# Kernel optimization log

Hardware: AMD Instinct MI355X
Metric: run time of the kernel (lower is better)

## Reference

```python
import jax, jax.numpy as jnp
import numpy as np

D_ATT = 1024
N_HEADS = 16
D_HEAD = D_ATT // N_HEADS


def _xavier(key, shape, scale):
    # xavier_uniform for Linear(d, d): limit = sqrt(6/(fan_in+fan_out))
    limit = float(np.sqrt(6.0 / (shape[0] + shape[1])))
    return jax.random.uniform(key, shape, jnp.float32, -limit, limit) * scale


def setup_inputs() -> dict:
    key = jax.random.key(0)
    ks = jax.random.split(key, 7)
    B, Lt, Ls = 2, 2048, 2048
    s = 1.0 / np.sqrt(D_ATT)
    return {
        "x_target": jax.random.normal(ks[0], (B, Lt, D_ATT), jnp.float32),
        "x_source": jax.random.normal(ks[1], (B, Ls, D_ATT), jnp.float32),
        "Wq": _xavier(ks[2], (D_ATT, D_ATT), s),  # torch Linear weight [out, in]
        "Wk": _xavier(ks[3], (D_ATT, D_ATT), s),
        "Wv": _xavier(ks[4], (D_ATT, D_ATT), s),
        "Wo": _xavier(ks[5], (D_ATT, D_ATT), 1.0),
        "bo": jax.random.uniform(ks[6], (D_ATT,), jnp.float32, -s, s),
    }


def reference(x_target, x_source, Wq, Wk, Wv, Wo, bo):
    B, Lt, _ = x_target.shape
    Ls = x_source.shape[1]
    H, Dh = N_HEADS, D_HEAD
    # projections (torch Linear: x @ W^T); RoPE defaults to identity
    Q = (x_target @ Wq.T).reshape(B, Lt, H, Dh)  # [B, Lt, H, Dh]
    K = (x_source @ Wk.T).reshape(B, Ls, H, Dh)
    V = (x_source @ Wv.T).reshape(B, Ls, H, Dh)
    scores = jnp.einsum("bthd,bshd->bhts", Q, K) / np.sqrt(Dh)
    attn = jax.nn.softmax(scores, axis=-1)
    out = jnp.einsum("bhts,bshd->bthd", attn, V).reshape(B, Lt, H * Dh)
    return out @ Wo.T + bo  # dropout p=0 -> identity
```

## Files before the change

### kernel.cpp

```cpp
#include <hip/hip_runtime.h>
#include <hip/hip_bf16.h>

typedef short bf16x8 __attribute__((ext_vector_type(8)));
typedef float f32x4 __attribute__((ext_vector_type(4)));

#define LDP 72

__device__ __forceinline__ float bf2f(ushort u) {
    union { unsigned int i; float f; } v; v.i = ((unsigned int)u) << 16; return v.f;
}
__device__ __forceinline__ ushort f2bf(float f) {
    union { float f; unsigned int i; } v; v.f = f;
    unsigned int x = v.i;
    x += 0x7fffu + ((x >> 16) & 1u);
    return (ushort)(x >> 16);
}

#define MFMA(a, b, c) __builtin_amdgcn_mfma_f32_16x16x32_bf16(a, b, c, 0, 0, 0)

__device__ __forceinline__ void gld_lds16(const ushort* g, ushort* l) {
    __builtin_amdgcn_global_load_lds(
        (const __attribute__((address_space(1))) unsigned int*)g,
        (__attribute__((address_space(3))) unsigned int*)l, 16, 0, 0);
}

#define WS_XT 0
#define WS_XS 4194304
#define WS_WQ 8388608
#define WS_WK 9437184
#define WS_WV 10485760
#define WS_WO 11534336
#define WS_QH 12582912
#define WS_KH 16777216
#define WS_VT 20971520
#define WS_AO 0

__global__ __launch_bounds__(256) void cast_bf16(
    const float* __restrict__ s0, const float* __restrict__ s1,
    const float* __restrict__ s2, const float* __restrict__ s3,
    const float* __restrict__ s4, const float* __restrict__ s5,
    ushort* __restrict__ ws)
{
    const int seg = blockIdx.y;
    const float* src = seg == 0 ? s0 : seg == 1 ? s1 : seg == 2 ? s2
                     : seg == 3 ? s3 : seg == 4 ? s4 : s5;
    const size_t off = seg == 0 ? WS_XT : seg == 1 ? WS_XS : seg == 2 ? WS_WQ
                     : seg == 3 ? WS_WK : seg == 4 ? WS_WV : (size_t)WS_WO;
    const int n4 = (seg < 2) ? 1048576 : 262144;
    ushort* d = ws + off;
    for (int i = blockIdx.x * 256 + threadIdx.x; i < n4; i += gridDim.x * 256) {
        float4 f = ((const float4*)src)[i];
        ushort4 u;
        u.x = f2bf(f.x); u.y = f2bf(f.y); u.z = f2bf(f.z); u.w = f2bf(f.w);
        ((ushort4*)d)[i] = u;
    }
}

__global__ __launch_bounds__(256) void gemm128(
    const ushort* __restrict__ xtb, const ushort* __restrict__ xsb,
    const ushort* __restrict__ wqb, const ushort* __restrict__ wkb,
    const ushort* __restrict__ wvb,
    ushort* __restrict__ qh, ushort* __restrict__ kh, ushort* __restrict__ vt)
{
    __shared__ __align__(16) ushort SM[16384];

    const int mode = blockIdx.z;
    const ushort* Ap = (mode == 0) ? xtb : xsb;
    const ushort* Wp = (mode == 0) ? wqb : (mode == 1 ? wkb : wvb);

    const int tid  = threadIdx.x;
    const int wave = tid >> 6, lane = tid & 63;
    const int quad = lane >> 4, lidx = lane & 15;
    const int wm = wave >> 1, wn = wave & 1;
    const int m0 = blockIdx.y * 128, n0 = blockIdx.x * 128;

    const int slr = lane >> 2, scb = lane & 3;
    auto stage = [&](int k0, int bufi) {
        ushort* Asb = SM + bufi * 4096;
        ushort* Bsb = SM + 8192 + bufi * 4096;
#pragma unroll
        for (int i2 = 0; i2 < 2; ++i2) {
            const int i = wave + i2 * 4;
            const int r = i * 16 + slr;
            gld_lds16(Ap + (size_t)(m0 + r) * 1024 + k0 + scb * 8, Asb + i * 512);
            gld_lds16(Wp + (size_t)(n0 + r) * 1024 + k0 + scb * 8, Bsb + i * 512);
        }
    };

    f32x4 acc[4][4] = {};
    stage(0, 0);
    __syncthreads();

    for (int kt = 0; kt < 32; ++kt) {
        const int cur = kt & 1;
        if (kt < 31) stage((kt + 1) * 32, cur ^ 1);
        const ushort* Asb = SM + cur * 4096;
        const ushort* Bsb = SM + 8192 + cur * 4096;
        bf16x8 af[4], bfr[4];
#pragma unroll
        for (int i = 0; i < 4; ++i) {
            af[i]  = *(const bf16x8*)(Asb + (wm * 64 + i * 16 + lidx) * 32 + quad * 8);
            bfr[i] = *(const bf16x8*)(Bsb + (wn * 64 + i * 16 + lidx) * 32 + quad * 8);
        }
#pragma unroll
        for (int mi = 0; mi < 4; ++mi)
#pragma unroll
            for (int ni = 0; ni < 4; ++ni)
                acc[mi][ni] = MFMA(af[mi], bfr[ni], acc[mi][ni]);
        __syncthreads();
    }

    if (mode == 2) {
        ushort* scr = SM + wave * 4096;
#pragma unroll
        for (int mi = 0; mi < 4; ++mi)
#pragma unroll
            for (int ni = 0; ni < 4; ++ni)
#pragma unroll
                for (int r = 0; r < 4; ++r) {
                    const int dl = ni * 16 + lidx;
                    const int tl = mi * 16 + quad * 4 + r;
                    const int col = (((tl >> 3) ^ (dl & 7)) << 3) | (tl & 7);
                    scr[dl * 64 + col] = f2bf(acc[mi][ni][r]);
                }
        asm volatile("s_waitcnt lgkmcnt(0)" ::: "memory");
        const int hh = (n0 + wn * 64) >> 6;
        const int bb = m0 >> 11;
        const int t0 = (m0 + wm * 64) & 2047;
        ushort* Vtp = vt + (size_t)(bb * 16 + hh) * 64 * 2048;
#pragma unroll
        for (int ii = 0; ii < 8; ++ii) {
            const int dl = ii * 8 + (lane >> 3);
            const int tb = lane & 7;
            uint4 vd = *(const uint4*)(scr + dl * 64 + ((tb ^ (dl & 7)) << 3));
            *(uint4*)(Vtp + (size_t)dl * 2048 + t0 + tb * 8) = vd;
        }
        return;
    }

#pragma unroll
    for (int mi = 0; mi < 4; ++mi)
#pragma unroll
        for (int ni = 0; ni < 4; ++ni)
#pragma unroll
            for (int r = 0; r < 4; ++r) {
                const int m = m0 + wm * 64 + mi * 16 + quad * 4 + r;
                const int n = n0 + wn * 64 + ni * 16 + lidx;
                const int b = m >> 11, t = m & 2047;
                const int h = n >> 6,  d = n & 63;
                ushort* dst = (mode == 0) ? qh : kh;
                dst[((size_t)(b * 16 + h) * 2048 + t) * 64 + d] = f2bf(acc[mi][ni][r]);
            }
}

__global__ __launch_bounds__(256) void gemm_out(
    const ushort* __restrict__ aob, const ushort* __restrict__ wob,
    const float* __restrict__ bias, float* __restrict__ outf)
{
    __shared__ __align__(16) ushort SM[12288];

    const int tid  = threadIdx.x;
    const int wave = tid >> 6, lane = tid & 63;
    const int quad = lane >> 4, lidx = lane & 15;
    const int m0 = blockIdx.y * 128, n0 = blockIdx.x * 64;

    const int slr = lane >> 2, scb = lane & 3;
    auto stage = [&](int k0, int bufi) {
        ushort* Asb = SM + bufi * 4096;
        ushort* Bsb = SM + 8192 + bufi * 2048;
#pragma unroll
        for (int i2 = 0; i2 < 2; ++i2) {
            const int i = wave * 2 + i2;
            gld_lds16(aob + (size_t)(m0 + i * 16 + slr) * 1024 + k0 + scb * 8,
                      Asb + i * 512);
        }
        gld_lds16(wob + (size_t)(n0 + wave * 16 + slr) * 1024 + k0 + scb * 8,
                  Bsb + wave * 512);
    };

    f32x4 acc[2][4] = {};
    stage(0, 0);
    __syncthreads();

    for (int kt = 0; kt < 32; ++kt) {
        const int cur = kt & 1;
        if (kt < 31) stage((kt + 1) * 32, cur ^ 1);
        const ushort* Asb = SM + cur * 4096;
        const ushort* Bsb = SM + 8192 + cur * 2048;
        bf16x8 af[2], bfr[4];
#pragma unroll
        for (int i = 0; i < 2; ++i)
            af[i] = *(const bf16x8*)(Asb + (wave * 32 + i * 16 + lidx) * 32 + quad * 8);
#pragma unroll
        for (int i = 0; i < 4; ++i)
            bfr[i] = *(const bf16x8*)(Bsb + (i * 16 + lidx) * 32 + quad * 8);
#pragma unroll
        for (int mi = 0; mi < 2; ++mi)
#pragma unroll
            for (int ni = 0; ni < 4; ++ni)
                acc[mi][ni] = MFMA(af[mi], bfr[ni], acc[mi][ni]);
        __syncthreads();
    }

#pragma unroll
    for (int mi = 0; mi < 2; ++mi)
#pragma unroll
        for (int ni = 0; ni < 4; ++ni)
#pragma unroll
            for (int r = 0; r < 4; ++r) {
                const int m = m0 + wave * 32 + mi * 16 + quad * 4 + r;
                const int n = n0 + ni * 16 + lidx;
                outf[(size_t)m * 1024 + n] = acc[mi][ni][r] + bias[n];
            }
}

__global__ __launch_bounds__(512) void flash_attn(
    const ushort* __restrict__ Qh, const ushort* __restrict__ Kh,
    const ushort* __restrict__ Vt, ushort* __restrict__ AO)
{
    __shared__ __align__(16) ushort Kb[2][4096];
    __shared__ __align__(16) ushort Vb[2][4096];
    __shared__ __align__(16) ushort P[8][16][LDP];

    const int tid  = threadIdx.x;
    const int wave = tid >> 6, lane = tid & 63;
    const int quad = lane >> 4, lidx = lane & 15;
    const int bh = blockIdx.y;
    const int b = bh >> 4, h = bh & 15;
    const int qbase = blockIdx.x * 128 + wave * 16;

    const ushort* Qp = Qh + (size_t)bh * 2048 * 64;
    const ushort* Kp = Kh + (size_t)bh * 2048 * 64;
    const ushort* Vp = Vt + (size_t)bh * 64 * 2048;

    bf16x8 q0, q1;
    {
        const ushort* qr = Qp + (size_t)(qbase + lidx) * 64 + quad * 8;
        union { ushort u[8]; uint4 v; } t0, t1;
        t0.v = *(const uint4*)qr;
        t1.v = *(const uint4*)(qr + 32);
#pragma unroll
        for (int i = 0; i < 8; ++i) {
            ((short*)&q0)[i] = (short)f2bf(bf2f(t0.u[i]) * 0.18033688f);
            ((short*)&q1)[i] = (short)f2bf(bf2f(t1.u[i]) * 0.18033688f);
        }
    }

    auto stage = [&](int s0, int bufi) {
        const int slot = wave * 64 + lane;
        const int r  = slot >> 3;
        const int bb = slot & 7;
        const int gb = bb ^ (r & 7);
        gld_lds16(Kp + (size_t)(s0 + r) * 64 + gb * 8, &Kb[bufi][wave * 512]);
        gld_lds16(Vp + (size_t)r * 2048 + s0 + gb * 8, &Vb[bufi][wave * 512]);
    };

    float lsum[4] = {};
    f32x4 o[4] = {};

    stage(0, 0);
    __syncthreads();

    for (int j = 0; j < 32; ++j) {
        const int cur = j & 1;
        stage(((j + 1) & 31) * 64, cur ^ 1);

        f32x4 s[4] = {};
#pragma unroll
        for (int n0 = 0; n0 < 4; ++n0) {
            const int row = n0 * 16 + lidx;
            bf16x8 k0 = *(const bf16x8*)&Kb[cur][row * 64 + ((quad ^ (row & 7)) * 8)];
            bf16x8 k1 = *(const bf16x8*)&Kb[cur][row * 64 + (((4 + quad) ^ (row & 7)) * 8)];
            s[n0] = MFMA(q0, k0, s[n0]);
            s[n0] = MFMA(q1, k1, s[n0]);
        }

#pragma unroll
        for (int n0 = 0; n0 < 4; ++n0)
#pragma unroll
            for (int r = 0; r < 4; ++r) {
                const float p = __builtin_amdgcn_exp2f(s[n0][r]);
                lsum[r] += p;
                P[wave][quad * 4 + r][n0 * 16 + lidx] = f2bf(p);
            }
        asm volatile("s_waitcnt lgkmcnt(0)" ::: "memory");
        bf16x8 p0 = *(const bf16x8*)&P[wave][lidx][quad * 8];
        bf16x8 p1 = *(const bf16x8*)&P[wave][lidx][32 + quad * 8];

#pragma unroll
        for (int n0 = 0; n0 < 4; ++n0) {
            const int d = n0 * 16 + lidx;
            bf16x8 v0 = *(const bf16x8*)&Vb[cur][d * 64 + ((quad ^ (d & 7)) * 8)];
            bf16x8 v1 = *(const bf16x8*)&Vb[cur][d * 64 + (((4 + quad) ^ (d & 7)) * 8)];
            o[n0] = MFMA(p0, v0, o[n0]);
            o[n0] = MFMA(p1, v1, o[n0]);
        }
        __syncthreads();
    }

#pragma unroll
    for (int r = 0; r < 4; ++r) {
        float v = lsum[r];
        v += __shfl_xor(v, 1);
        v += __shfl_xor(v, 2);
        v += __shfl_xor(v, 4);
        v += __shfl_xor(v, 8);
        lsum[r] = v;
    }

#pragma unroll
    for (int n0 = 0; n0 < 4; ++n0)
#pragma unroll
        for (int r = 0; r < 4; ++r) {
            const int tt = qbase + quad * 4 + r;
            const int d  = n0 * 16 + lidx;
            AO[(size_t)(b * 2048 + tt) * 1024 + h * 64 + d] =
                f2bf(o[n0][r] / lsum[r]);
        }
}

extern "C" void kernel_launch(void* const* d_in, const int* in_sizes, int n_in,
                              void* d_out, int out_size, void* d_ws, size_t ws_size,
                              hipStream_t stream) {
    const float* xt = (const float*)d_in[0];
    const float* xs = (const float*)d_in[1];
    const float* Wq = (const float*)d_in[2];
    const float* Wk = (const float*)d_in[3];
    const float* Wv = (const float*)d_in[4];
    const float* Wo = (const float*)d_in[5];
    const float* bo = (const float*)d_in[6];
    float* out = (float*)d_out;

    ushort* ws = (ushort*)d_ws;

    cast_bf16<<<dim3(1024, 6, 1), 256, 0, stream>>>(xt, xs, Wq, Wk, Wv, Wo, ws);

    gemm128<<<dim3(8, 32, 3), 256, 0, stream>>>(
        ws + WS_XT, ws + WS_XS, ws + WS_WQ, ws + WS_WK, ws + WS_WV,
        ws + WS_QH, ws + WS_KH, ws + WS_VT);

    flash_attn<<<dim3(16, 32, 1), 512, 0, stream>>>(
        ws + WS_QH, ws + WS_KH, ws + WS_VT, ws + WS_AO);

    gemm_out<<<dim3(16, 32, 1), 256, 0, stream>>>(
        ws + WS_AO, ws + WS_WO, bo, out);
}
```

Measured before the change: 217.1 us.

## Process two 16-row query tiles per wave in flash attention

Each wave now handles 32 query rows as two 16-row tiles, so every K/V fragment read from LDS feeds twice as many MFMAs and K/V staging traffic per query is halved. The grid shrinks to 256 blocks of 256 queries. Softmax probabilities and outputs are now converted with a packed bf16x2 intrinsic. The cost is more registers per wave and fewer blocks (256 on a 256-CU part), which reduces latency hiding and occupancy.

```diff
diff --git a/kernel.cpp b/kernel.cpp
--- a/kernel.cpp
+++ b/kernel.cpp
@@ -14,6 +14,11 @@
     unsigned int x = v.i;
     x += 0x7fffu + ((x >> 16) & 1u);
     return (ushort)(x >> 16);
+}
+__device__ __forceinline__ ushort2 pk2bf(float a, float b) {
+    union { __hip_bfloat162 h2; ushort2 u2; } cv;
+    cv.h2 = __float22bfloat162_rn(float2{a, b});
+    return cv.u2;
 }
 
 #define MFMA(a, b, c) __builtin_amdgcn_mfma_f32_16x16x32_bf16(a, b, c, 0, 0, 0)
@@ -227,22 +232,23 @@
     const int quad = lane >> 4, lidx = lane & 15;
     const int bh = blockIdx.y;
     const int b = bh >> 4, h = bh & 15;
-    const int qbase = blockIdx.x * 128 + wave * 16;
+    const int qbase = blockIdx.x * 256 + wave * 32;
 
     const ushort* Qp = Qh + (size_t)bh * 2048 * 64;
     const ushort* Kp = Kh + (size_t)bh * 2048 * 64;
     const ushort* Vp = Vt + (size_t)bh * 64 * 2048;
 
-    bf16x8 q0, q1;
-    {
-        const ushort* qr = Qp + (size_t)(qbase + lidx) * 64 + quad * 8;
+    bf16x8 q[2][2];
+#pragma unroll
+    for (int t = 0; t < 2; ++t) {
+        const ushort* qr = Qp + (size_t)(qbase + t * 16 + lidx) * 64 + quad * 8;
         union { ushort u[8]; uint4 v; } t0, t1;
         t0.v = *(const uint4*)qr;
         t1.v = *(const uint4*)(qr + 32);
 #pragma unroll
         for (int i = 0; i < 8; ++i) {
-            ((short*)&q0)[i] = (short)f2bf(bf2f(t0.u[i]) * 0.18033688f);
-            ((short*)&q1)[i] = (short)f2bf(bf2f(t1.u[i]) * 0.18033688f);
+            ((short*)&q[t][0])[i] = (short)f2bf(bf2f(t0.u[i]) * 0.18033688f);
+            ((short*)&q[t][1])[i] = (short)f2bf(bf2f(t1.u[i]) * 0.18033688f);
         }
     }
 
@@ -255,8 +261,8 @@
         gld_lds16(Vp + (size_t)r * 2048 + s0 + gb * 8, &Vb[bufi][wave * 512]);
     };
 
-    float lsum[4] = {};
-    f32x4 o[4] = {};
+    float lsum[2][4] = {};
+    f32x4 o[2][4] = {};
 
     stage(0, 0);
     __syncthreads();
@@ -265,58 +271,78 @@
         const int cur = j & 1;
         stage(((j + 1) & 31) * 64, cur ^ 1);
 
-        f32x4 s[4] = {};
+        f32x4 s[2][4] = {};
 #pragma unroll
         for (int n0 = 0; n0 < 4; ++n0) {
             const int row = n0 * 16 + lidx;
             bf16x8 k0 = *(const bf16x8*)&Kb[cur][row * 64 + ((quad ^ (row & 7)) * 8)];
             bf16x8 k1 = *(const bf16x8*)&Kb[cur][row * 64 + (((4 + quad) ^ (row & 7)) * 8)];
-            s[n0] = MFMA(q0, k0, s[n0]);
-            s[n0] = MFMA(q1, k1, s[n0]);
-        }
-
-#pragma unroll
-        for (int n0 = 0; n0 < 4; ++n0)
-#pragma unroll
-            for (int r = 0; r < 4; ++r) {
-                const float p = __builtin_amdgcn_exp2f(s[n0][r]);
-                lsum[r] += p;
-                P[wave][quad * 4 + r][n0 * 16 + lidx] = f2bf(p);
-            }
-        asm volatile("s_waitcnt lgkmcnt(0)" ::: "memory");
-        bf16x8 p0 = *(const bf16x8*)&P[wave][lidx][quad * 8];
-        bf16x8 p1 = *(const bf16x8*)&P[wave][lidx][32 + quad * 8];
+#pragma unroll
+            for (int t = 0; t < 2; ++t) {
+                s[t][n0] = MFMA(q[t][0], k0, s[t][n0]);
+                s[t][n0] = MFMA(q[t][1], k1, s[t][n0]);
+            }
+        }
+
+        bf16x8 pf[2][2];
+#pragma unroll
+        for (int t = 0; t < 2; ++t) {
+#pragma unroll
+            for (int n0 = 0; n0 < 4; ++n0)
+#pragma unroll
+                for (int r = 0; r < 4; r += 2) {
+                    const float pa = __builtin_amdgcn_exp2f(s[t][n0][r]);
+                    const float pb = __builtin_amdgcn_exp2f(s[t][n0][r + 1]);
+                    lsum[t][r] += pa;
+                    lsum[t][r + 1] += pb;
+                    const ushort2 u2 = pk2bf(pa, pb);
+                    P[wave][quad * 4 + r][n0 * 16 + lidx] = u2.x;
+                    P[wave][quad * 4 + r + 1][n0 * 16 + lidx] = u2.y;
+                }
+            asm volatile("s_waitcnt lgkmcnt(0)" ::: "memory");
+            pf[t][0] = *(const bf16x8*)&P[wave][lidx][quad * 8];
+            pf[t][1] = *(const bf16x8*)&P[wave][lidx][32 + quad * 8];
+        }
 
 #pragma unroll
         for (int n0 = 0; n0 < 4; ++n0) {
             const int d = n0 * 16 + lidx;
             bf16x8 v0 = *(const bf16x8*)&Vb[cur][d * 64 + ((quad ^ (d & 7)) * 8)];
             bf16x8 v1 = *(const bf16x8*)&Vb[cur][d * 64 + (((4 + quad) ^ (d & 7)) * 8)];
-            o[n0] = MFMA(p0, v0, o[n0]);
-            o[n0] = MFMA(p1, v1, o[n0]);
+#pragma unroll
+            for (int t = 0; t < 2; ++t) {
+                o[t][n0] = MFMA(pf[t][0], v0, o[t][n0]);
+                o[t][n0] = MFMA(pf[t][1], v1, o[t][n0]);
+            }
         }
         __syncthreads();
     }
 
 #pragma unroll
-    for (int r = 0; r < 4; ++r) {
-        float v = lsum[r];
-        v += __shfl_xor(v, 1);
-        v += __shfl_xor(v, 2);
-        v += __shfl_xor(v, 4);
-        v += __shfl_xor(v, 8);
-        lsum[r] = v;
-    }
-
-#pragma unroll
-    for (int n0 = 0; n0 < 4; ++n0)
+    for (int t = 0; t < 2; ++t)
 #pragma unroll
         for (int r = 0; r < 4; ++r) {
-            const int tt = qbase + quad * 4 + r;
-            const int d  = n0 * 16 + lidx;
-            AO[(size_t)(b * 2048 + tt) * 1024 + h * 64 + d] =
-                f2bf(o[n0][r] / lsum[r]);
-        }
+            float v = lsum[t][r];
+            v += __shfl_xor(v, 1);
+            v += __shfl_xor(v, 2);
+            v += __shfl_xor(v, 4);
+            v += __shfl_xor(v, 8);
+            lsum[t][r] = v;
+        }
+
+#pragma unroll
+    for (int t = 0; t < 2; ++t)
+#pragma unroll
+        for (int n0 = 0; n0 < 4; ++n0)
+#pragma unroll
+            for (int r = 0; r < 4; r += 2) {
+                const int tt = qbase + t * 16 + quad * 4 + r;
+                const int d  = n0 * 16 + lidx;
+                const ushort2 u2 = pk2bf(o[t][n0][r] / lsum[t][r],
+                                         o[t][n0][r + 1] / lsum[t][r + 1]);
+                AO[(size_t)(b * 2048 + tt) * 1024 + h * 64 + d] = u2.x;
+                AO[(size_t)(b * 2048 + tt + 1) * 1024 + h * 64 + d] = u2.y;
+            }
 }
 
 extern "C" void kernel_launch(void* const* d_in, const int* in_sizes, int n_in,
@@ -339,7 +365,7 @@
         ws + WS_XT, ws + WS_XS, ws + WS_WQ, ws + WS_WK, ws + WS_WV,
         ws + WS_QH, ws + WS_KH, ws + WS_VT);
 
-    flash_attn<<<dim3(16, 32, 1), 512, 0, stream>>>(
+    flash_attn<<<dim3(8, 32, 1), 512, 0, stream>>>(
         ws + WS_QH, ws + WS_KH, ws + WS_VT, ws + WS_AO);
 
     gemm_out<<<dim3(16, 32, 1), 256, 0, stream>>>(
```

New measurement: 220.8 us. Within noise of the previous version (+1.7%).

## Triple-buffer GEMM LDS stages with single barrier and stage Q/K stores via LDS

Applied to the files above, without the earlier changes.

Both projection GEMMs and the output GEMM move from double-buffered to triple-buffered LDS staging. Loads are issued two tiles ahead, and a vmcnt-bounded wait plus one barrier replaces the two __syncthreads per k-step. The Q/K epilogue now writes through a swizzled LDS scratch so each lane stores 16-byte vectors instead of scattered 2-byte values. The cost is more LDS per block, which may lower occupancy, and wrap-around dummy loads on the last iterations.

```diff
diff --git a/kernel.cpp b/kernel.cpp
--- a/kernel.cpp
+++ b/kernel.cpp
@@ -17,6 +17,8 @@
 }
 
 #define MFMA(a, b, c) __builtin_amdgcn_mfma_f32_16x16x32_bf16(a, b, c, 0, 0, 0)
+
+#define WAIT_BARRIER(N) asm volatile("s_waitcnt vmcnt(" #N ")\n\ts_barrier" ::: "memory")
 
 __device__ __forceinline__ void gld_lds16(const ushort* g, ushort* l) {
     __builtin_amdgcn_global_load_lds(
@@ -62,7 +64,7 @@
     const ushort* __restrict__ wvb,
     ushort* __restrict__ qh, ushort* __restrict__ kh, ushort* __restrict__ vt)
 {
-    __shared__ __align__(16) ushort SM[16384];
+    __shared__ __align__(16) ushort SM[24576];
 
     const int mode = blockIdx.z;
     const ushort* Ap = (mode == 0) ? xtb : xsb;
@@ -77,7 +79,7 @@
     const int slr = lane >> 2, scb = lane & 3;
     auto stage = [&](int k0, int bufi) {
         ushort* Asb = SM + bufi * 4096;
-        ushort* Bsb = SM + 8192 + bufi * 4096;
+        ushort* Bsb = SM + 12288 + bufi * 4096;
 #pragma unroll
         for (int i2 = 0; i2 < 2; ++i2) {
             const int i = wave + i2 * 4;
@@ -89,13 +91,14 @@
 
     f32x4 acc[4][4] = {};
     stage(0, 0);
-    __syncthreads();
+    stage(32, 1);
 
     for (int kt = 0; kt < 32; ++kt) {
-        const int cur = kt & 1;
-        if (kt < 31) stage((kt + 1) * 32, cur ^ 1);
+        const int cur = kt % 3;
+        WAIT_BARRIER(4);
+        stage(((kt + 2) & 31) * 32, (kt + 2) % 3);
         const ushort* Asb = SM + cur * 4096;
-        const ushort* Bsb = SM + 8192 + cur * 4096;
+        const ushort* Bsb = SM + 12288 + cur * 4096;
         bf16x8 af[4], bfr[4];
 #pragma unroll
         for (int i = 0; i < 4; ++i) {
@@ -107,11 +110,12 @@
 #pragma unroll
             for (int ni = 0; ni < 4; ++ni)
                 acc[mi][ni] = MFMA(af[mi], bfr[ni], acc[mi][ni]);
-        __syncthreads();
-    }
+    }
+    __syncthreads();
+
+    ushort* scr = SM + wave * 4096;
 
     if (mode == 2) {
-        ushort* scr = SM + wave * 4096;
 #pragma unroll
         for (int mi = 0; mi < 4; ++mi)
 #pragma unroll
@@ -144,20 +148,33 @@
         for (int ni = 0; ni < 4; ++ni)
 #pragma unroll
             for (int r = 0; r < 4; ++r) {
-                const int m = m0 + wm * 64 + mi * 16 + quad * 4 + r;
-                const int n = n0 + wn * 64 + ni * 16 + lidx;
-                const int b = m >> 11, t = m & 2047;
-                const int h = n >> 6,  d = n & 63;
-                ushort* dst = (mode == 0) ? qh : kh;
-                dst[((size_t)(b * 16 + h) * 2048 + t) * 64 + d] = f2bf(acc[mi][ni][r]);
+                const int tl = mi * 16 + quad * 4 + r;
+                const int dl = ni * 16 + lidx;
+                const int col = (((dl >> 3) ^ (tl & 7)) << 3) | (dl & 7);
+                scr[tl * 64 + col] = f2bf(acc[mi][ni][r]);
             }
+    asm volatile("s_waitcnt lgkmcnt(0)" ::: "memory");
+    {
+        ushort* dst = (mode == 0) ? qh : kh;
+        const int hh = (n0 + wn * 64) >> 6;
+        const int bb = m0 >> 11;
+        const int tbase = (m0 + wm * 64) & 2047;
+        ushort* Hp = dst + (size_t)(bb * 16 + hh) * 2048 * 64;
+#pragma unroll
+        for (int ii = 0; ii < 8; ++ii) {
+            const int tl = ii * 8 + (lane >> 3);
+            const int c  = lane & 7;
+            uint4 vd = *(const uint4*)(scr + tl * 64 + ((c ^ (tl & 7)) << 3));
+            *(uint4*)(Hp + (size_t)(tbase + tl) * 64 + c * 8) = vd;
+        }
+    }
 }
 
 __global__ __launch_bounds__(256) void gemm_out(
     const ushort* __restrict__ aob, const ushort* __restrict__ wob,
     const float* __restrict__ bias, float* __restrict__ outf)
 {
-    __shared__ __align__(16) ushort SM[12288];
+    __shared__ __align__(16) ushort SM[18432];
 
     const int tid  = threadIdx.x;
     const int wave = tid >> 6, lane = tid & 63;
@@ -167,7 +184,7 @@
     const int slr = lane >> 2, scb = lane & 3;
     auto stage = [&](int k0, int bufi) {
         ushort* Asb = SM + bufi * 4096;
-        ushort* Bsb = SM + 8192 + bufi * 2048;
+        ushort* Bsb = SM + 12288 + bufi * 2048;
 #pragma unroll
         for (int i2 = 0; i2 < 2; ++i2) {
             const int i = wave * 2 + i2;
@@ -180,13 +197,14 @@
 
     f32x4 acc[2][4] = {};
     stage(0, 0);
-    __syncthreads();
+    stage(32, 1);
 
     for (int kt = 0; kt < 32; ++kt) {
-        const int cur = kt & 1;
-        if (kt < 31) stage((kt + 1) * 32, cur ^ 1);
+        const int cur = kt % 3;
+        WAIT_BARRIER(3);
+        stage(((kt + 2) & 31) * 32, (kt + 2) % 3);
         const ushort* Asb = SM + cur * 4096;
-        const ushort* Bsb = SM + 8192 + cur * 2048;
+        const ushort* Bsb = SM + 12288 + cur * 2048;
         bf16x8 af[2], bfr[4];
 #pragma unroll
         for (int i = 0; i < 2; ++i)
@@ -199,7 +217,6 @@
 #pragma unroll
             for (int ni = 0; ni < 4; ++ni)
                 acc[mi][ni] = MFMA(af[mi], bfr[ni], acc[mi][ni]);
-        __syncthreads();
     }
 
 #pragma unroll
```

New measurement: 206.4 us. 1.05x faster.
